# Kernel optimization log

Measured on AMD Instinct MI355X. Metric: run time of the kernel, lower is better.

Reference implementation:

```python
import jax, jax.numpy as jnp
import numpy as np

B, S, D, H, E, K = 4, 2048, 1024, 2048, 8, 2
TEMP = 5.0
EPS = 1e-9


def setup_inputs() -> dict:
    key = jax.random.key(0)
    k_x, k_wg, k_w1, k_w2 = jax.random.split(key, 4)
    scale = 0.02
    return {
        "x": jax.random.normal(k_x, (B, S, D), dtype=jnp.float32),
        "Wg": jax.random.normal(k_wg, (D, E), dtype=jnp.float32) * scale,
        "bg": jnp.zeros((E,), dtype=jnp.float32),
        "W1": jax.random.normal(k_w1, (E, D, H), dtype=jnp.float32) * scale,
        "b1": jnp.zeros((E, H), dtype=jnp.float32),
        "W2": jax.random.normal(k_w2, (E, H, D), dtype=jnp.float32) * scale,
        "b2": jnp.zeros((E, D), dtype=jnp.float32),
    }


def reference(x, Wg, bg, W1, b1, W2, b2):
    # Gating: softmax over experts with temperature
    logits = jnp.einsum('bsd,de->bse', x, Wg) + bg  # [B,S,E]
    probs = jax.nn.softmax(logits / TEMP, axis=-1)
    # Top-k mask, renormalized (zeros for non-selected experts)
    vals, idx = jax.lax.top_k(probs, K)              # [B,S,K]
    onehot = jax.nn.one_hot(idx, E, dtype=x.dtype)   # [B,S,K,E]
    mask = jnp.einsum('bske,bsk->bse', onehot, vals) # scatter topk values
    gates = mask / (jnp.sum(mask, axis=-1, keepdims=True) + EPS)
    # Expert FFNs (dense over experts; gate weight is exactly 0 for unrouted)
    h = jax.nn.gelu(jnp.einsum('bsd,edh->besh', x, W1) + b1[None, :, None, :],
                    approximate=False)               # [B,E,S,H]
    out = jnp.einsum('besh,ehd->besd', h, W2) + b2[None, :, None, :]
    y = jnp.einsum('bse,besd->bsd', gates, out)      # weighted combine
    return y
```

## Files before the change

kernel.cpp:

```cpp
#include <hip/hip_runtime.h>
#include <stdint.h>

#define NTOK 8192
#define DIM  1024
#define HID  2048
#define NE   8
#define CAP  17408
#define TM 128
#define TN 128
#define TKK 64

typedef __bf16  bf16x8  __attribute__((ext_vector_type(8)));
typedef float   floatx4 __attribute__((ext_vector_type(4)));

__device__ __forceinline__ unsigned short f2bf(float f) {
  union { float f; unsigned u; } v; v.f = f;
  unsigned r = v.u + 0x7FFFu + ((v.u >> 16) & 1u);
  return (unsigned short)(r >> 16);
}

__device__ __forceinline__ void async_ld16(const unsigned short* g, unsigned short* l) {
  __builtin_amdgcn_global_load_lds(
      (const __attribute__((address_space(1))) unsigned int*)(const void*)g,
      (__attribute__((address_space(3))) unsigned int*)(void*)l, 16, 0, 0);
}

__device__ __forceinline__ float gelu_fast(float v) {
  float g = 0.79788456080286536f * (v + 0.044715f * v * v * v);
  float t = __builtin_amdgcn_exp2f(-2.8853900817779268f * g);
  return v * __builtin_amdgcn_rcpf(1.0f + t);
}

__device__ __forceinline__ uint2 pack4bf(float a, float b, float c, float d) {
  uint2 o;
  o.x = (unsigned)f2bf(a) | ((unsigned)f2bf(b) << 16);
  o.y = (unsigned)f2bf(c) | ((unsigned)f2bf(d) << 16);
  return o;
}

__global__ __launch_bounds__(256)
void transpose_all_kernel(const float* __restrict__ W1, const float* __restrict__ W2,
                          unsigned short* __restrict__ w1t, unsigned short* __restrict__ w2t,
                          int* __restrict__ meta, unsigned short* __restrict__ zbuf) {
  __shared__ unsigned short T[64][65];
  int z = blockIdx.z;
  int tid = threadIdx.x;
  if (z == 0 && blockIdx.x == 0 && blockIdx.y == 0) {
    if (tid < 48) meta[tid] = 0;
    uint2 zz = {0u, 0u};
    *(uint2*)&zbuf[tid * 4] = zz;
  }
  const float* S;
  unsigned short* D2;
  int R, C, c0, r0;
  if (z < 8) {
    S = W1 + (size_t)z * DIM * HID;
    D2 = w1t + (size_t)z * DIM * HID;
    R = DIM; C = HID; c0 = blockIdx.x * 64; r0 = blockIdx.y * 64;
  } else {
    S = W2 + (size_t)(z - 8) * DIM * HID;
    D2 = w2t + (size_t)(z - 8) * DIM * HID;
    R = HID; C = DIM; c0 = blockIdx.y * 64; r0 = blockIdx.x * 64;
  }
  int lr = tid >> 4;
  int lc = (tid & 15) * 4;
#pragma unroll
  for (int i = 0; i < 4; i++) {
    int r = lr + i * 16;
    float4 v = *(const float4*)&S[(size_t)(r0 + r) * C + c0 + lc];
    T[lc + 0][r] = f2bf(v.x);
    T[lc + 1][r] = f2bf(v.y);
    T[lc + 2][r] = f2bf(v.z);
    T[lc + 3][r] = f2bf(v.w);
  }
  __syncthreads();
  int sc = tid >> 3;
  int sr = (tid & 7) * 8;
#pragma unroll
  for (int i = 0; i < 2; i++) {
    int c = sc + i * 32;
    const unsigned short* p = &T[c][sr];
    uint4 o;
    o.x = (unsigned)p[0] | ((unsigned)p[1] << 16);
    o.y = (unsigned)p[2] | ((unsigned)p[3] << 16);
    o.z = (unsigned)p[4] | ((unsigned)p[5] << 16);
    o.w = (unsigned)p[6] | ((unsigned)p[7] << 16);
    *(uint4*)&D2[(size_t)(c0 + c) * R + r0 + sr] = o;
  }
}

__global__ __launch_bounds__(256)
void gating_kernel(const float* __restrict__ x, const float* __restrict__ Wg,
                   const float* __restrict__ bg, int* __restrict__ tok_e,
                   float* __restrict__ tok_g, unsigned short* __restrict__ xb,
                   int* __restrict__ cnt) {
  __shared__ float WgS[NE * DIM];
  __shared__ int ghist[NE];
  int tid = threadIdx.x;
  if (tid < NE) ghist[tid] = 0;
#pragma unroll
  for (int j = 0; j < NE * DIM / 256; j++) {
    int i = j * 256 + tid;
    WgS[(i & 7) * DIM + (i >> 3)] = Wg[i];
  }
  __syncthreads();
  int wave = tid >> 6;
  int lane = tid & 63;
#pragma unroll
  for (int ti = 0; ti < 2; ti++) {
    int t = blockIdx.x * 8 + wave * 2 + ti;
    const float* xr = x + (size_t)t * DIM;
    float p[NE];
#pragma unroll
    for (int e = 0; e < NE; e++) p[e] = 0.f;
#pragma unroll
    for (int it = 0; it < DIM / 256; it++) {
      int d = (it * 64 + lane) * 4;
      float4 xv = *(const float4*)&xr[d];
      *(uint2*)&xb[(size_t)t * DIM + d] = pack4bf(xv.x, xv.y, xv.z, xv.w);
#pragma unroll
      for (int e = 0; e < NE; e++) {
        float4 wv = *(const float4*)&WgS[e * DIM + d];
        p[e] += xv.x * wv.x + xv.y * wv.y + xv.z * wv.z + xv.w * wv.w;
      }
    }
#pragma unroll
    for (int e = 0; e < NE; e++) {
#pragma unroll
      for (int off = 32; off > 0; off >>= 1) p[e] += __shfl_xor(p[e], off);
    }
    if (lane == 0) {
      float s[NE];
      float m = -1e30f;
#pragma unroll
      for (int e = 0; e < NE; e++) { s[e] = (p[e] + bg[e]) * 0.2f; m = fmaxf(m, s[e]); }
      float sum = 0.f;
#pragma unroll
      for (int e = 0; e < NE; e++) { s[e] = expf(s[e] - m); sum += s[e]; }
      float inv = 1.0f / sum;
      int i0 = 0; float v0 = -1.f;
#pragma unroll
      for (int e = 0; e < NE; e++) { float pe = s[e] * inv; if (pe > v0) { v0 = pe; i0 = e; } }
      int i1 = -1; float v1 = -1.f;
#pragma unroll
      for (int e = 0; e < NE; e++) {
        if (e == i0) continue;
        float pe = s[e] * inv; if (pe > v1) { v1 = pe; i1 = e; }
      }
      float den = v0 + v1 + 1e-9f;
      tok_e[t * 2]     = i0; tok_g[t * 2]     = v0 / den;
      tok_e[t * 2 + 1] = i1; tok_g[t * 2 + 1] = v1 / den;
      atomicAdd(&ghist[i0], 1);
      atomicAdd(&ghist[i1], 1);
    }
  }
  __syncthreads();
  if (tid < NE) atomicAdd(&cnt[tid], ghist[tid]);
}

__global__ __launch_bounds__(256)
void route_kernel(const int* __restrict__ tok_e, const float* __restrict__ tok_g,
                  const int* __restrict__ cnt, int* __restrict__ cnt2,
                  int* __restrict__ seg_out,
                  int* __restrict__ token_row, float* __restrict__ gate_row,
                  int* __restrict__ tok_pos) {
  __shared__ int hist[NE];
  __shared__ int base[NE];
  __shared__ int segs[NE + 1];
  __shared__ int cnts[NE];
  int tid = threadIdx.x;
  if (tid < NE) { hist[tid] = 0; cnts[tid] = cnt[tid]; }
  __syncthreads();
  if (tid == 0) {
    int s = 0;
    for (int e = 0; e < NE; e++) { segs[e] = s; s += ((cnts[e] + TM - 1) / TM) * TM; }
    segs[NE] = s;
  }
  __syncthreads();
  int t = blockIdx.x * 256 + tid;
  int e0 = tok_e[t * 2];
  int e1 = tok_e[t * 2 + 1];
  int r0 = atomicAdd(&hist[e0], 1);
  int r1 = atomicAdd(&hist[e1], 1);
  __syncthreads();
  if (tid < NE) base[tid] = atomicAdd(&cnt2[tid], hist[tid]);
  __syncthreads();
  int p0 = segs[e0] + base[e0] + r0;
  int p1 = segs[e1] + base[e1] + r1;
  token_row[p0] = t; gate_row[p0] = tok_g[t * 2];     tok_pos[t * 2]     = p0;
  token_row[p1] = t; gate_row[p1] = tok_g[t * 2 + 1]; tok_pos[t * 2 + 1] = p1;
  if (tid <= NE) seg_out[tid] = segs[tid];
#pragma unroll
  for (int e = 0; e < NE; e++)
    for (int i = segs[e] + cnts[e] + tid; i < segs[e + 1]; i += 256) {
      token_row[i] = -1;
      gate_row[i] = 0.f;
    }
}

__global__ __launch_bounds__(256, 3)
void gemm1_kernel(const unsigned short* __restrict__ xb, const unsigned short* __restrict__ w1t,
                  const float* __restrict__ b1, const int* __restrict__ token_row,
                  const int* __restrict__ seg, const unsigned short* __restrict__ zbuf,
                  unsigned short* __restrict__ hbuf) {
  __shared__ __align__(16) unsigned short As[TM * TKK];
  __shared__ __align__(16) unsigned short Bs[TN * TKK];
  int row0 = blockIdx.y * TM;
  int total = seg[NE];
  if (row0 >= total) return;
  int e = 0;
  while (row0 >= seg[e + 1]) e++;
  int n0 = blockIdx.x * TN;
  int tid = threadIdx.x;
  int lane = tid & 63;
  int w = tid >> 6;
  int wm = w >> 1;
  int wn = w & 1;
  int lrow = lane >> 3;
  int lk   = (lane & 7) * 8;

  floatx4 zero4 = {0.f, 0.f, 0.f, 0.f};
  floatx4 acc[4][4];
#pragma unroll
  for (int a = 0; a < 4; a++)
#pragma unroll
    for (int b = 0; b < 4; b++) acc[a][b] = zero4;

  const unsigned short* w1e = w1t + (size_t)e * DIM * HID;
  const unsigned short* srcA[4];
  const unsigned short* srcB[4];
#pragma unroll
  for (int i = 0; i < 4; i++) {
    int r = w * 32 + i * 8 + lrow;
    int t = token_row[row0 + r];
    srcA[i] = (t >= 0 ? xb + (size_t)t * DIM : zbuf) + lk;
  }
#pragma unroll
  for (int i = 0; i < 4; i++) {
    int r = w * 32 + i * 8 + lrow;
    srcB[i] = w1e + (size_t)(n0 + r) * DIM + lk;
  }

  int mr = lane & 15;
  int kq = (lane >> 4) * 8;

  for (int k0 = 0; k0 < DIM; k0 += TKK) {
#pragma unroll
    for (int i = 0; i < 4; i++)
      async_ld16(srcA[i] + k0, &As[(w * 32 + i * 8 + lrow) * TKK + lk]);
#pragma unroll
    for (int i = 0; i < 4; i++)
      async_ld16(srcB[i] + k0, &Bs[(w * 32 + i * 8 + lrow) * TKK + lk]);
    __syncthreads();
#pragma unroll
    for (int kk = 0; kk < TKK; kk += 32) {
      bf16x8 af[4], bfr[4];
#pragma unroll
      for (int im = 0; im < 4; im++)
        af[im] = *(const bf16x8*)&As[(wm * 64 + im * 16 + mr) * TKK + kk + kq];
#pragma unroll
      for (int in = 0; in < 4; in++)
        bfr[in] = *(const bf16x8*)&Bs[(wn * 64 + in * 16 + mr) * TKK + kk + kq];
#pragma unroll
      for (int im = 0; im < 4; im++)
#pragma unroll
        for (int in = 0; in < 4; in++)
          acc[im][in] = __builtin_amdgcn_mfma_f32_16x16x32_bf16(bfr[in], af[im], acc[im][in], 0, 0, 0);
    }
    __syncthreads();
  }
  int quad = lane >> 4;
  int c16 = lane & 15;
  const float* b1e = b1 + e * HID;
#pragma unroll
  for (int im = 0; im < 4; im++) {
    int r = row0 + wm * 64 + im * 16 + c16;
#pragma unroll
    for (int in = 0; in < 4; in++) {
      int c = n0 + wn * 64 + in * 16 + quad * 4;
      float4 bias = *(const float4*)&b1e[c];
      float v0 = gelu_fast(acc[im][in][0] + bias.x);
      float v1 = gelu_fast(acc[im][in][1] + bias.y);
      float v2 = gelu_fast(acc[im][in][2] + bias.z);
      float v3 = gelu_fast(acc[im][in][3] + bias.w);
      *(uint2*)&hbuf[(size_t)r * HID + c] = pack4bf(v0, v1, v2, v3);
    }
  }
}

__global__ __launch_bounds__(256, 3)
void gemm2_kernel(const unsigned short* __restrict__ hbuf, const unsigned short* __restrict__ w2t,
                  const float* __restrict__ b2, const float* __restrict__ gate_row,
                  const int* __restrict__ seg, unsigned short* __restrict__ obuf) {
  __shared__ __align__(16) unsigned short As[TM * TKK];
  __shared__ __align__(16) unsigned short Bs[TN * TKK];
  int row0 = blockIdx.y * TM;
  int total = seg[NE];
  if (row0 >= total) return;
  int e = 0;
  while (row0 >= seg[e + 1]) e++;
  int n0 = blockIdx.x * TN;
  int tid = threadIdx.x;
  int lane = tid & 63;
  int w = tid >> 6;
  int wm = w >> 1;
  int wn = w & 1;
  int lrow = lane >> 3;
  int lk   = (lane & 7) * 8;

  floatx4 zero4 = {0.f, 0.f, 0.f, 0.f};
  floatx4 acc[4][4];
#pragma unroll
  for (int a = 0; a < 4; a++)
#pragma unroll
    for (int b = 0; b < 4; b++) acc[a][b] = zero4;

  const unsigned short* w2e = w2t + (size_t)e * DIM * HID;
  const unsigned short* srcA[4];
  const unsigned short* srcB[4];
#pragma unroll
  for (int i = 0; i < 4; i++) {
    int r = w * 32 + i * 8 + lrow;
    srcA[i] = hbuf + (size_t)(row0 + r) * HID + lk;
  }
#pragma unroll
  for (int i = 0; i < 4; i++) {
    int r = w * 32 + i * 8 + lrow;
    srcB[i] = w2e + (size_t)(n0 + r) * HID + lk;
  }

  int mr = lane & 15;
  int kq = (lane >> 4) * 8;

  for (int k0 = 0; k0 < HID; k0 += TKK) {
#pragma unroll
    for (int i = 0; i < 4; i++)
      async_ld16(srcA[i] + k0, &As[(w * 32 + i * 8 + lrow) * TKK + lk]);
#pragma unroll
    for (int i = 0; i < 4; i++)
      async_ld16(srcB[i] + k0, &Bs[(w * 32 + i * 8 + lrow) * TKK + lk]);
    __syncthreads();
#pragma unroll
    for (int kk = 0; kk < TKK; kk += 32) {
      bf16x8 af[4], bfr[4];
#pragma unroll
      for (int im = 0; im < 4; im++)
        af[im] = *(const bf16x8*)&As[(wm * 64 + im * 16 + mr) * TKK + kk + kq];
#pragma unroll
      for (int in = 0; in < 4; in++)
        bfr[in] = *(const bf16x8*)&Bs[(wn * 64 + in * 16 + mr) * TKK + kk + kq];
#pragma unroll
      for (int im = 0; im < 4; im++)
#pragma unroll
        for (int in = 0; in < 4; in++)
          acc[im][in] = __builtin_amdgcn_mfma_f32_16x16x32_bf16(bfr[in], af[im], acc[im][in], 0, 0, 0);
    }
    __syncthreads();
  }
  int quad = lane >> 4;
  int c16 = lane & 15;
  const float* b2e = b2 + e * DIM;
#pragma unroll
  for (int im = 0; im < 4; im++) {
    int r = row0 + wm * 64 + im * 16 + c16;
    float gs = gate_row[r];
#pragma unroll
    for (int in = 0; in < 4; in++) {
      int c = n0 + wn * 64 + in * 16 + quad * 4;
      float4 bias = *(const float4*)&b2e[c];
      float v0 = gs * (acc[im][in][0] + bias.x);
      float v1 = gs * (acc[im][in][1] + bias.y);
      float v2 = gs * (acc[im][in][2] + bias.z);
      float v3 = gs * (acc[im][in][3] + bias.w);
      *(uint2*)&obuf[(size_t)r * DIM + c] = pack4bf(v0, v1, v2, v3);
    }
  }
}

__global__ void combine_kernel(const unsigned short* __restrict__ obuf,
                               const int* __restrict__ tok_pos,
                               float* __restrict__ y) {
  int idx = blockIdx.x * 256 + threadIdx.x;
  int t = idx >> 7;
  int c = (idx & 127) << 3;
  int p0 = tok_pos[t * 2];
  int p1 = tok_pos[t * 2 + 1];
  uint4 a = *(const uint4*)(obuf + (size_t)p0 * DIM + c);
  uint4 b = *(const uint4*)(obuf + (size_t)p1 * DIM + c);
  float out[8];
  unsigned au[4] = {a.x, a.y, a.z, a.w};
  unsigned bu[4] = {b.x, b.y, b.z, b.w};
#pragma unroll
  for (int i = 0; i < 4; i++) {
    union { unsigned u; float f; } lo0, hi0, lo1, hi1;
    lo0.u = au[i] << 16; hi0.u = au[i] & 0xFFFF0000u;
    lo1.u = bu[i] << 16; hi1.u = bu[i] & 0xFFFF0000u;
    out[i * 2]     = lo0.f + lo1.f;
    out[i * 2 + 1] = hi0.f + hi1.f;
  }
  float* yp = y + (size_t)t * DIM + c;
  *(float4*)yp       = *(float4*)&out[0];
  *(float4*)(yp + 4) = *(float4*)&out[4];
}

extern "C" void kernel_launch(void* const* d_in, const int* in_sizes, int n_in,
                              void* d_out, int out_size, void* d_ws, size_t ws_size,
                              hipStream_t stream) {
  const float* x  = (const float*)d_in[0];
  const float* Wg = (const float*)d_in[1];
  const float* bg = (const float*)d_in[2];
  const float* W1 = (const float*)d_in[3];
  const float* b1 = (const float*)d_in[4];
  const float* W2 = (const float*)d_in[5];
  const float* b2 = (const float*)d_in[6];
  float* y = (float*)d_out;
  char* ws = (char*)d_ws;

  constexpr size_t OFF_META = 0;
  constexpr size_t OFF_TOKE = 256;
  constexpr size_t OFF_TOKG = OFF_TOKE + (size_t)NTOK * 2 * 4;
  constexpr size_t OFF_TPOS = OFF_TOKG + (size_t)NTOK * 2 * 4;
  constexpr size_t OFF_TROW = OFF_TPOS + (size_t)NTOK * 2 * 4;
  constexpr size_t OFF_GROW = OFF_TROW + (size_t)CAP * 4;
  constexpr size_t OFF_ZB   = OFF_GROW + (size_t)CAP * 4;
  constexpr size_t OFF_XB   = OFF_ZB  + (size_t)DIM * 2;
  constexpr size_t OFF_W1T  = OFF_XB  + (size_t)NTOK * DIM * 2;
  constexpr size_t OFF_W2T  = OFF_W1T + (size_t)NE * DIM * HID * 2;
  constexpr size_t OFF_H    = OFF_W2T + (size_t)NE * DIM * HID * 2;
  constexpr size_t OFF_OBUF = OFF_XB;

  int* cnt        = (int*)(ws + OFF_META);
  int* cnt2       = (int*)(ws + OFF_META + 64);
  int* seg        = (int*)(ws + OFF_META + 128);
  int* tok_e      = (int*)(ws + OFF_TOKE);
  float* tok_g    = (float*)(ws + OFF_TOKG);
  int* tok_pos    = (int*)(ws + OFF_TPOS);
  int* token_row  = (int*)(ws + OFF_TROW);
  float* gate_row = (float*)(ws + OFF_GROW);
  unsigned short* zbuf = (unsigned short*)(ws + OFF_ZB);
  unsigned short* xb   = (unsigned short*)(ws + OFF_XB);
  unsigned short* w1t  = (unsigned short*)(ws + OFF_W1T);
  unsigned short* w2t  = (unsigned short*)(ws + OFF_W2T);
  unsigned short* hbuf = (unsigned short*)(ws + OFF_H);
  unsigned short* obuf = (unsigned short*)(ws + OFF_OBUF);

  transpose_all_kernel<<<dim3(32, 16, 16), 256, 0, stream>>>(W1, W2, w1t, w2t, (int*)(ws + OFF_META), zbuf);
  gating_kernel<<<NTOK / 8, 256, 0, stream>>>(x, Wg, bg, tok_e, tok_g, xb, cnt);
  route_kernel<<<NTOK / 256, 256, 0, stream>>>(tok_e, tok_g, cnt, cnt2, seg, token_row, gate_row, tok_pos);
  gemm1_kernel<<<dim3(HID / TN, CAP / TM), 256, 0, stream>>>(xb, w1t, b1, token_row, seg, zbuf, hbuf);
  gemm2_kernel<<<dim3(DIM / TN, CAP / TM), 256, 0, stream>>>(hbuf, w2t, b2, gate_row, seg, obuf);
  combine_kernel<<<NTOK * DIM / 8 / 256, 256, 0, stream>>>(obuf, tok_pos, y);
}
```

Measured before the change: 437.4 us.

## Merge weight transpose and gating into one prep kernel with swizzled LDS

Folds the weight-transpose and gating kernels into a single launch: the first 1024 blocks do gating and the remaining 8192 blocks transpose W1/W2 tiles to bf16. The transpose now packs four rows per thread and writes into an XOR-swizzled LDS tile, which cuts bank conflicts and per-element stores. The meta counters are zeroed with a memset instead of inside the transpose kernel. This saves one launch boundary and lets gating overlap with the transpose. In exchange, every block reserves the full 32KB gating shared buffer, which can lower occupancy for the transpose blocks.

```diff
diff --git a/kernel.cpp b/kernel.cpp
--- a/kernel.cpp
+++ b/kernel.cpp
@@ -38,65 +38,70 @@
   return o;
 }
 
+__device__ __forceinline__ void transpose_tile64(const float* S, unsigned short* D2,
+                                                 int R, int C, int r0, int c0,
+                                                 unsigned short* Ts, int tid) {
+  int rr = tid >> 4;
+  int cc = (tid & 15) * 4;
+  float4 v0 = *(const float4*)&S[(size_t)(r0 + rr * 4 + 0) * C + c0 + cc];
+  float4 v1 = *(const float4*)&S[(size_t)(r0 + rr * 4 + 1) * C + c0 + cc];
+  float4 v2 = *(const float4*)&S[(size_t)(r0 + rr * 4 + 2) * C + c0 + cc];
+  float4 v3 = *(const float4*)&S[(size_t)(r0 + rr * 4 + 3) * C + c0 + cc];
+  uint2 p0 = pack4bf(v0.x, v1.x, v2.x, v3.x);
+  uint2 p1 = pack4bf(v0.y, v1.y, v2.y, v3.y);
+  uint2 p2 = pack4bf(v0.z, v1.z, v2.z, v3.z);
+  uint2 p3 = pack4bf(v0.w, v1.w, v2.w, v3.w);
+  char* tb = (char*)Ts;
+  int rb = rr * 8;
+#pragma unroll
+  for (int j = 0; j < 4; j++) {
+    int col = cc + j;
+    uint2 pj = j == 0 ? p0 : j == 1 ? p1 : j == 2 ? p2 : p3;
+    *(uint2*)(tb + col * 128 + (rb ^ ((col & 7) << 4))) = pj;
+  }
+  __syncthreads();
+  int sr = (tid & 7) * 8;
+#pragma unroll
+  for (int i = 0; i < 2; i++) {
+    int col = (tid >> 3) + i * 32;
+    uint4 o = *(const uint4*)(tb + col * 128 + ((sr * 2) ^ ((col & 7) << 4)));
+    *(uint4*)&D2[(size_t)(c0 + col) * R + r0 + sr] = o;
+  }
+}
+
 __global__ __launch_bounds__(256)
-void transpose_all_kernel(const float* __restrict__ W1, const float* __restrict__ W2,
-                          unsigned short* __restrict__ w1t, unsigned short* __restrict__ w2t,
-                          int* __restrict__ meta, unsigned short* __restrict__ zbuf) {
-  __shared__ unsigned short T[64][65];
-  int z = blockIdx.z;
+void prep_kernel(const float* __restrict__ x, const float* __restrict__ Wg,
+                 const float* __restrict__ bg, const float* __restrict__ W1,
+                 const float* __restrict__ W2,
+                 unsigned short* __restrict__ w1t, unsigned short* __restrict__ w2t,
+                 int* __restrict__ tok_e, float* __restrict__ tok_g,
+                 unsigned short* __restrict__ xb, int* __restrict__ cnt,
+                 unsigned short* __restrict__ zbuf) {
+  __shared__ __align__(16) char smem[NE * DIM * 4];
+  __shared__ int ghist[NE];
+  int bid = blockIdx.x;
   int tid = threadIdx.x;
-  if (z == 0 && blockIdx.x == 0 && blockIdx.y == 0) {
-    if (tid < 48) meta[tid] = 0;
-    uint2 zz = {0u, 0u};
-    *(uint2*)&zbuf[tid * 4] = zz;
-  }
-  const float* S;
-  unsigned short* D2;
-  int R, C, c0, r0;
-  if (z < 8) {
-    S = W1 + (size_t)z * DIM * HID;
-    D2 = w1t + (size_t)z * DIM * HID;
-    R = DIM; C = HID; c0 = blockIdx.x * 64; r0 = blockIdx.y * 64;
-  } else {
-    S = W2 + (size_t)(z - 8) * DIM * HID;
-    D2 = w2t + (size_t)(z - 8) * DIM * HID;
-    R = HID; C = DIM; c0 = blockIdx.y * 64; r0 = blockIdx.x * 64;
-  }
-  int lr = tid >> 4;
-  int lc = (tid & 15) * 4;
-#pragma unroll
-  for (int i = 0; i < 4; i++) {
-    int r = lr + i * 16;
-    float4 v = *(const float4*)&S[(size_t)(r0 + r) * C + c0 + lc];
-    T[lc + 0][r] = f2bf(v.x);
-    T[lc + 1][r] = f2bf(v.y);
-    T[lc + 2][r] = f2bf(v.z);
-    T[lc + 3][r] = f2bf(v.w);
-  }
-  __syncthreads();
-  int sc = tid >> 3;
-  int sr = (tid & 7) * 8;
-#pragma unroll
-  for (int i = 0; i < 2; i++) {
-    int c = sc + i * 32;
-    const unsigned short* p = &T[c][sr];
-    uint4 o;
-    o.x = (unsigned)p[0] | ((unsigned)p[1] << 16);
-    o.y = (unsigned)p[2] | ((unsigned)p[3] << 16);
-    o.z = (unsigned)p[4] | ((unsigned)p[5] << 16);
-    o.w = (unsigned)p[6] | ((unsigned)p[7] << 16);
-    *(uint4*)&D2[(size_t)(c0 + c) * R + r0 + sr] = o;
-  }
-}
-
-__global__ __launch_bounds__(256)
-void gating_kernel(const float* __restrict__ x, const float* __restrict__ Wg,
-                   const float* __restrict__ bg, int* __restrict__ tok_e,
-                   float* __restrict__ tok_g, unsigned short* __restrict__ xb,
-                   int* __restrict__ cnt) {
-  __shared__ float WgS[NE * DIM];
-  __shared__ int ghist[NE];
-  int tid = threadIdx.x;
+
+  if (bid >= 1024) {
+    unsigned short* Ts = (unsigned short*)smem;
+    int tz = bid - 1024;
+    if (tz < 4096) {
+      if (tz == 0) { uint2 zz = {0u, 0u}; *(uint2*)&zbuf[tid * 4] = zz; }
+      int e = tz >> 9, t = tz & 511;
+      int c0 = (t & 31) * 64, r0 = (t >> 5) * 64;
+      transpose_tile64(W1 + (size_t)e * DIM * HID, w1t + (size_t)e * DIM * HID,
+                       DIM, HID, r0, c0, Ts, tid);
+    } else {
+      int tz2 = tz - 4096;
+      int e = tz2 >> 9, t = tz2 & 511;
+      int r0 = (t & 31) * 64, c0 = (t >> 5) * 64;
+      transpose_tile64(W2 + (size_t)e * DIM * HID, w2t + (size_t)e * DIM * HID,
+                       HID, DIM, r0, c0, Ts, tid);
+    }
+    return;
+  }
+
+  float* WgS = (float*)smem;
   if (tid < NE) ghist[tid] = 0;
 #pragma unroll
   for (int j = 0; j < NE * DIM / 256; j++) {
@@ -108,7 +113,7 @@
   int lane = tid & 63;
 #pragma unroll
   for (int ti = 0; ti < 2; ti++) {
-    int t = blockIdx.x * 8 + wave * 2 + ti;
+    int t = bid * 8 + wave * 2 + ti;
     const float* xr = x + (size_t)t * DIM;
     float p[NE];
 #pragma unroll
@@ -444,8 +449,10 @@
   unsigned short* hbuf = (unsigned short*)(ws + OFF_H);
   unsigned short* obuf = (unsigned short*)(ws + OFF_OBUF);
 
-  transpose_all_kernel<<<dim3(32, 16, 16), 256, 0, stream>>>(W1, W2, w1t, w2t, (int*)(ws + OFF_META), zbuf);
-  gating_kernel<<<NTOK / 8, 256, 0, stream>>>(x, Wg, bg, tok_e, tok_g, xb, cnt);
+  hipMemsetAsync(ws, 0, 192, stream);
+
+  prep_kernel<<<1024 + 8192, 256, 0, stream>>>(x, Wg, bg, W1, W2, w1t, w2t,
+                                               tok_e, tok_g, xb, cnt, zbuf);
   route_kernel<<<NTOK / 256, 256, 0, stream>>>(tok_e, tok_g, cnt, cnt2, seg, token_row, gate_row, tok_pos);
   gemm1_kernel<<<dim3(HID / TN, CAP / TM), 256, 0, stream>>>(xb, w1t, b1, token_row, seg, zbuf, hbuf);
   gemm2_kernel<<<dim3(DIM / TN, CAP / TM), 256, 0, stream>>>(hbuf, w2t, b2, gate_row, seg, obuf);
```

Result: no change. 432.0 us (-1.2%).
